# Optimization experiments

Measured on AMD Instinct MI355X. Metric: run time of the kernel, lower is better.

Reference implementation:

```python
import jax, jax.numpy as jnp
import numpy as np

D_MODEL = 1024
N_HEADS = 16
D_K = D_MODEL // N_HEADS
LOCAL_WINDOW = 128
GLOBAL_TOKENS = 16


def sparse_mask(seq_len):
    i = jnp.arange(seq_len)[:, None]
    j = jnp.arange(seq_len)[None, :]
    local = jnp.abs(i - j) <= LOCAL_WINDOW
    glob = (i < GLOBAL_TOKENS) | (j < GLOBAL_TOKENS)
    causal = j <= i
    return ((local | glob) & causal)[None, None]  # [1,1,S,S]


def setup_inputs() -> dict:
    key = jax.random.key(0)
    ks = jax.random.split(key, 11)
    B, S = 2, 2048
    std = 1.0 / np.sqrt(D_MODEL)
    inp = {
        'query': jax.random.normal(ks[0], (B, S, D_MODEL), jnp.float32),
        'key': jax.random.normal(ks[1], (B, S, D_MODEL), jnp.float32),
        'value': jax.random.normal(ks[2], (B, S, D_MODEL), jnp.float32),
        'w_q': jax.random.normal(ks[3], (D_MODEL, D_MODEL), jnp.float32) * std,
        'b_q': jnp.zeros((D_MODEL,), jnp.float32),
        'w_k': jax.random.normal(ks[4], (D_MODEL, D_MODEL), jnp.float32) * std,
        'b_k': jnp.zeros((D_MODEL,), jnp.float32),
        'w_v': jax.random.normal(ks[5], (D_MODEL, D_MODEL), jnp.float32) * std,
        'b_v': jnp.zeros((D_MODEL,), jnp.float32),
        'w_o': jax.random.normal(ks[6], (D_MODEL, D_MODEL), jnp.float32) * std,
        'b_o': jnp.zeros((D_MODEL,), jnp.float32),
    }
    return inp


def reference(query, key, value, w_q, b_q, w_k, b_k, w_v, b_v, w_o, b_o):
    B, S, _ = query.shape
    # project and split heads -> [B,H,S,d_k]
    def proj(x, w, b):
        y = x @ w.T + b
        return y.reshape(B, S, N_HEADS, D_K).transpose(0, 2, 1, 3)
    q = proj(query, w_q, b_q)
    k = proj(key, w_k, b_k)
    v = proj(value, w_v, b_v)
    scores = jnp.einsum('bhqd,bhkd->bhqk', q, k) / np.sqrt(D_K).astype(np.float32)
    mask = sparse_mask(S)
    scores = jnp.where(mask, scores, -jnp.inf)
    attn = jax.nn.softmax(scores, axis=-1)
    out = jnp.einsum('bhqk,bhkd->bhqd', attn, v)
    out = out.transpose(0, 2, 1, 3).reshape(B, S, D_MODEL)
    return out @ w_o.T + b_o
```

## Files before the change

kernel.cpp:

```cpp
#include <hip/hip_runtime.h>

typedef unsigned short u16;
typedef u16 u16x8 __attribute__((ext_vector_type(8)));
typedef __bf16 bf16x8 __attribute__((ext_vector_type(8)));
typedef float f32x4 __attribute__((ext_vector_type(4)));

#define MFMA16 __builtin_amdgcn_mfma_f32_16x16x32_bf16

__device__ __forceinline__ u16 f2bf(float f) {
  unsigned u = __builtin_bit_cast(unsigned, f);
  u += 0x7FFFu + ((u >> 16) & 1u);
  return (u16)(u >> 16);
}

__device__ __forceinline__ int swz(int row, int bcol) {
  return row * 128 + (bcol ^ ((row & 7) << 4));
}

__device__ __forceinline__ void gl16(const u16* g, u16* l) {
  __builtin_amdgcn_global_load_lds(
      (const __attribute__((address_space(1))) unsigned int*)g,
      (__attribute__((address_space(3))) unsigned int*)l, 16, 0, 0);
}

__device__ __forceinline__ void BARR() {
  asm volatile("" ::: "memory");
  __builtin_amdgcn_s_barrier();
  asm volatile("" ::: "memory");
}
#define VMCNT(n) asm volatile("s_waitcnt vmcnt(" #n ")" ::: "memory")
#define LGKM0 asm volatile("s_waitcnt lgkmcnt(0)" ::: "memory")

__global__ __launch_bounds__(256)
void cast_all(const float* __restrict__ q, const float* __restrict__ k,
              const float* __restrict__ v, const float* __restrict__ wq,
              const float* __restrict__ wk, const float* __restrict__ wv,
              const float* __restrict__ wo, u16* __restrict__ ws) {
  const long i = ((long)blockIdx.x * 256 + threadIdx.x) * 8;
  const float* s;
  u16* d;
  if (i < 12582912) {
    const int seg = (int)(i >> 22);
    const float* xs = (seg == 0) ? q : (seg == 1) ? k : v;
    s = xs + (i & 4194303);
    d = ws + 4194304 + i;
  } else {
    const long j = i - 12582912;
    const int seg = (int)(j >> 20);
    const float* wsrc = (seg == 0) ? wq : (seg == 1) ? wk : (seg == 2) ? wv : wo;
    s = wsrc + (j & 1048575);
    d = ws + j;
  }
  float4 v0 = *(const float4*)s;
  float4 v1 = *(const float4*)(s + 4);
  u16x8 p = {f2bf(v0.x), f2bf(v0.y), f2bf(v0.z), f2bf(v0.w),
             f2bf(v1.x), f2bf(v1.y), f2bf(v1.z), f2bf(v1.w)};
  *(u16x8*)d = p;
}

#define OSTGA(tt, c, j)                                                     \
  gl16(Ain + (m0 + (c)*64 + (w << 4) + (j)*8 + (lane >> 3)) * 1024 +        \
           (tt)*64 + (((lane & 7) ^ (lane >> 3)) << 3),                     \
       (u16*)(sb + (((tt)&1) << 15) + (c)*8192 + (w << 11) + ((j) << 10)))
#define OSTGB(tt, c, j)                                                     \
  gl16(W + (n0 + (c)*64 + (w << 4) + (j)*8 + (lane >> 3)) * 1024 +          \
           (tt)*64 + (((lane & 7) ^ (lane >> 3)) << 3),                     \
       (u16*)(sb + (((tt)&1) << 15) + 16384 + (c)*8192 + (w << 11) +        \
              ((j) << 10)))
#define OLDA()                                                              \
  _Pragma("unroll") for (int m = 0; m < 4; ++m) {                           \
    char* p = sb + bo + rowAb + m * 16 * 128;                               \
    af[0][m] = __builtin_bit_cast(bf16x8, *(const u16x8*)(p + colr0));      \
    af[1][m] = __builtin_bit_cast(bf16x8, *(const u16x8*)(p + colr1));      \
  }
#define OLDB(n)                                                             \
  {                                                                         \
    char* p = sb + bo + rowBb + (n)*16 * 128;                               \
    bf[0][n] = __builtin_bit_cast(bf16x8, *(const u16x8*)(p + colr0));      \
    bf[1][n] = __builtin_bit_cast(bf16x8, *(const u16x8*)(p + colr1));      \
  }
#define OFMA(nh)                                                            \
  __builtin_amdgcn_s_setprio(1);                                            \
  _Pragma("unroll") for (int m = 0; m < 4; ++m)                             \
  _Pragma("unroll") for (int n = 0; n < 2; ++n) {                           \
    acc[m][(nh)*2 + n] =                                                    \
        MFMA16(af[0][m], bf[0][(nh)*2 + n], acc[m][(nh)*2 + n], 0, 0, 0);   \
    acc[m][(nh)*2 + n] =                                                    \
        MFMA16(af[1][m], bf[1][(nh)*2 + n], acc[m][(nh)*2 + n], 0, 0, 0);   \
  }                                                                         \
  __builtin_amdgcn_s_setprio(0);

__device__ __forceinline__ void core128(const u16* __restrict__ Ain,
                                        const u16* __restrict__ W, int m0,
                                        int n0, char* sb,
                                        f32x4 (&acc)[4][4]) {
  const int tid = threadIdx.x, lane = tid & 63, w = tid >> 6;
  const int wm = w >> 1, wn = w & 1;
  const int r = lane & 15, g = lane >> 4;
  bf16x8 af[2][4], bf[2][4];

  const int colr0 = (g * 16) ^ ((r & 7) << 4);
  const int colr1 = (64 + g * 16) ^ ((r & 7) << 4);
  const int rowAb = (wm * 64 + r) * 128;
  const int rowBb = 16384 + (wn * 64 + r) * 128;

#pragma unroll
  for (int c = 0; c < 2; ++c) { OSTGA(0, c, 0); OSTGA(0, c, 1); }
#pragma unroll
  for (int c = 0; c < 2; ++c) { OSTGB(0, c, 0); OSTGB(0, c, 1); }
#pragma unroll
  for (int c = 0; c < 2; ++c) { OSTGA(1, c, 0); OSTGA(1, c, 1); }
  VMCNT(4);
  __builtin_amdgcn_s_barrier();
  asm volatile("" ::: "memory");

  for (int t = 0; t < 16; ++t) {
    const int bo = (t & 1) << 15;
    if (t < 15) { OSTGB(t + 1, 0, 0); OSTGB(t + 1, 0, 1); OSTGB(t + 1, 1, 0); OSTGB(t + 1, 1, 1); }
    OLDA();
    OLDB(0); OLDB(1);
    OFMA(0);
    BARR();
    if (t < 14) { OSTGA(t + 2, 0, 0); OSTGA(t + 2, 0, 1); OSTGA(t + 2, 1, 0); OSTGA(t + 2, 1, 1); }
    OLDB(2); OLDB(3);
    OFMA(1);
    if (t < 14) { VMCNT(4); } else if (t == 14) { VMCNT(0); }
    BARR();
  }
}

__global__ __launch_bounds__(256)
void qkv_gemm128(const u16* __restrict__ ws_in, const float* __restrict__ c0,
                 const float* __restrict__ c1, const float* __restrict__ c2,
                 u16* __restrict__ o0, u16* __restrict__ o1,
                 u16* __restrict__ o2) {
  const int bid = blockIdx.x;
  const int s = (bid & 7) * 96 + (bid >> 3);
  const int z = s >> 8;
  const int rem = s & 255;
  const int m0 = (rem >> 3) << 7, n0 = (rem & 7) << 7;

  const u16* __restrict__ Ain = ws_in + 4194304 + z * 4194304;
  const u16* __restrict__ W = ws_in + z * 1048576;
  const float* Bi = (z == 0) ? c0 : (z == 1) ? c1 : c2;
  u16* O = (z == 0) ? o0 : (z == 1) ? o1 : o2;

  const int tid = threadIdx.x, lane = tid & 63, w = tid >> 6;
  const int wm = w >> 1, wn = w & 1;
  const int r = lane & 15, g = lane >> 4;

  __shared__ u16 SH[32768];
  f32x4 acc[4][4] = {};
  core128(Ain, W, m0, n0, (char*)SH, acc);

#pragma unroll
  for (int n = 0; n < 4; ++n) {
    const int gn = n0 + wn * 64 + n * 16 + r;
    const int hh = gn >> 6, d = gn & 63;
    const float bv = Bi[gn];
#pragma unroll
    for (int m = 0; m < 4; ++m) {
#pragma unroll
      for (int q = 0; q < 4; ++q) {
        int gm = m0 + wm * 64 + m * 16 + g * 4 + q;
        int bb = gm >> 11, sIdx = gm & 2047;
        O[((bb * 16 + hh) * 2048 + sIdx) * 64 + d] = f2bf(acc[m][n][q] + bv);
      }
    }
  }
}

__global__ __launch_bounds__(256)
void out_gemm_p(const u16* __restrict__ Ain2, const u16* __restrict__ W2,
                const float* __restrict__ Bi, float* __restrict__ C) {
  const int bid = blockIdx.x;
  const int s = (bid & 7) * 32 + (bid >> 3);
  const int m0 = (s >> 3) << 7, n0 = (s & 7) << 7;

  const int tid = threadIdx.x, lane = tid & 63, w = tid >> 6;
  const int wm = w >> 1, wn = w & 1;
  const int r = lane & 15, g = lane >> 4;

  __shared__ u16 SH[32768];
  f32x4 acc[4][4] = {};
  core128(Ain2, W2, m0, n0, (char*)SH, acc);

#pragma unroll
  for (int m = 0; m < 4; ++m) {
#pragma unroll
    for (int n = 0; n < 4; ++n) {
      int gn = n0 + wn * 64 + n * 16 + r;
      float bv = Bi[gn];
#pragma unroll
      for (int q = 0; q < 4; ++q) {
        int gm = m0 + wm * 64 + m * 16 + g * 4 + q;
        C[gm * 1024 + gn] = acc[m][n][q] + bv;
      }
    }
  }
}

__global__ __launch_bounds__(256)
void attn_kernel(const u16* __restrict__ Q, const u16* __restrict__ K,
                 const u16* __restrict__ V, u16* __restrict__ O) {
  const int qt = blockIdx.x, h = blockIdx.y, b = blockIdx.z;
  const int tid = threadIdx.x, lane = tid & 63, w = tid >> 6;
  const int r = lane & 15, g = lane >> 4;
  const int q0 = qt * 64;
  const int base = (b * 16 + h) * 131072;
  const u16* Qb = Q + base;

  __shared__ u16 Ks[2][4096];
  __shared__ u16 Vt[2][4096];
  __shared__ u16 Pl[4608];

  bf16x8 qf[2];
  {
    const u16* qp = Qb + (q0 + w * 16 + r) * 64 + g * 8;
    qf[0] = __builtin_bit_cast(bf16x8, *(const u16x8*)qp);
    qf[1] = __builtin_bit_cast(bf16x8, *(const u16x8*)(qp + 32));
  }

  f32x4 acc[4] = {};
  float m_run[4] = {-1e30f, -1e30f, -1e30f, -1e30f};
  float l_run[4] = {};

  const int nt = (qt <= 3) ? (qt + 1) : 4;
  const int srow = tid >> 3, sc = (tid & 7) * 8;
  const u16* Kg = K + base + srow * 64 + sc;
  const u16* Vg = V + base + srow * 64 + sc;

  u16x8 krA[2], vrA[2], krB[2], vrB[2];
  krA[0] = *(const u16x8*)(Kg);
  krA[1] = *(const u16x8*)(Kg + 2048);
  vrA[0] = *(const u16x8*)(Vg);
  vrA[1] = *(const u16x8*)(Vg + 2048);

#pragma unroll
  for (int tix = 0; tix < 4; ++tix) {
    if (tix < nt) {
      const int j0 = ((tix == 0) ? 0 : ((qt <= 3) ? tix : (qt - 3 + tix))) * 64;
      const int bo = (tix & 1) * 8192;
      if ((tix & 1) == 0) {
#pragma unroll
        for (int i = 0; i < 2; ++i) {
          int row = i * 32 + srow;
          *(u16x8*)((char*)Ks + bo + swz(row, sc * 2)) = krA[i];
#pragma unroll
          for (int qq = 0; qq < 8; ++qq) {
            int d = sc + qq;
            *(u16*)((char*)Vt + bo + d * 128 + ((2 * row) ^ ((d & 7) << 4))) =
                vrA[i][qq];
          }
        }
      } else {
#pragma unroll
        for (int i = 0; i < 2; ++i) {
          int row = i * 32 + srow;
          *(u16x8*)((char*)Ks + bo + swz(row, sc * 2)) = krB[i];
#pragma unroll
          for (int qq = 0; qq < 8; ++qq) {
            int d = sc + qq;
            *(u16*)((char*)Vt + bo + d * 128 + ((2 * row) ^ ((d & 7) << 4))) =
                vrB[i][qq];
          }
        }
      }
      if (tix + 1 < nt) {
        const int jn = (((qt <= 3) ? (tix + 1) : (qt - 2 + tix)) * 64) * 64;
        if ((tix & 1) == 0) {
          krB[0] = *(const u16x8*)(Kg + jn);
          krB[1] = *(const u16x8*)(Kg + jn + 2048);
          vrB[0] = *(const u16x8*)(Vg + jn);
          vrB[1] = *(const u16x8*)(Vg + jn + 2048);
        } else {
          krA[0] = *(const u16x8*)(Kg + jn);
          krA[1] = *(const u16x8*)(Kg + jn + 2048);
          vrA[0] = *(const u16x8*)(Vg + jn);
          vrA[1] = *(const u16x8*)(Vg + jn + 2048);
        }
      }
      LGKM0;
      BARR();

      f32x4 S[4] = {};
#pragma unroll
      for (int kk = 0; kk < 2; ++kk)
#pragma unroll
        for (int n = 0; n < 4; ++n) {
          bf16x8 kf = __builtin_bit_cast(
              bf16x8, *(const u16x8*)((char*)Ks + bo +
                                      swz(n * 16 + r, kk * 64 + g * 16)));
          S[n] = MFMA16(qf[kk], kf, S[n], 0, 0, 0);
        }

      float mloc[4] = {-1e30f, -1e30f, -1e30f, -1e30f};
#pragma unroll
      for (int n = 0; n < 4; ++n) {
        int j = j0 + n * 16 + r;
#pragma unroll
        for (int q = 0; q < 4; ++q) {
          int i = q0 + w * 16 + g * 4 + q;
          bool ok = (j <= i) && (((i - j) <= 128) || (j < 16));
          float s = ok ? S[n][q] * 0.125f : -1e30f;
          S[n][q] = s;
          mloc[q] = fmaxf(mloc[q], s);
        }
      }
#pragma unroll
      for (int q = 0; q < 4; ++q)
#pragma unroll
        for (int off = 1; off < 16; off <<= 1)
          mloc[q] = fmaxf(mloc[q], __shfl_xor(mloc[q], off));

      float alpha[4], rsum[4] = {};
#pragma unroll
      for (int q = 0; q < 4; ++q) {
        float mn = fmaxf(m_run[q], mloc[q]);
        alpha[q] = __expf(m_run[q] - mn);
        m_run[q] = mn;
      }
#pragma unroll
      for (int n = 0; n < 4; ++n)
#pragma unroll
        for (int q = 0; q < 4; ++q) {
          float p = __expf(S[n][q] - m_run[q]);
          S[n][q] = p;
          rsum[q] += p;
        }
#pragma unroll
      for (int q = 0; q < 4; ++q) {
#pragma unroll
        for (int off = 1; off < 16; off <<= 1)
          rsum[q] += __shfl_xor(rsum[q], off);
        l_run[q] = l_run[q] * alpha[q] + rsum[q];
      }
#pragma unroll
      for (int n = 0; n < 4; ++n) {
        acc[n][0] *= alpha[0];
        acc[n][1] *= alpha[1];
        acc[n][2] *= alpha[2];
        acc[n][3] *= alpha[3];
      }

#pragma unroll
      for (int n = 0; n < 4; ++n)
#pragma unroll
        for (int q = 0; q < 4; ++q)
          *((u16*)((char*)Pl + w * 2304 + (g * 4 + q) * 144) + (n * 16 + r)) =
              f2bf(S[n][q]);

#pragma unroll
      for (int kk = 0; kk < 2; ++kk) {
        bf16x8 pf = __builtin_bit_cast(
            bf16x8, *(const u16x8*)((char*)Pl + w * 2304 + r * 144 + kk * 64 +
                                    g * 16));
#pragma unroll
        for (int n = 0; n < 4; ++n) {
          bf16x8 vf = __builtin_bit_cast(
              bf16x8, *(const u16x8*)((char*)Vt + bo +
                                      swz(n * 16 + r, kk * 64 + g * 16)));
          acc[n] = MFMA16(pf, vf, acc[n], 0, 0, 0);
        }
      }
    }
  }

#pragma unroll
  for (int n = 0; n < 4; ++n)
#pragma unroll
    for (int q = 0; q < 4; ++q) {
      int s = q0 + w * 16 + g * 4 + q;
      int d = n * 16 + r;
      O[(b * 2048 + s) * 1024 + h * 64 + d] = f2bf(acc[n][q] / l_run[q]);
    }
}

extern "C" void kernel_launch(void* const* d_in, const int* in_sizes, int n_in,
                              void* d_out, int out_size, void* d_ws,
                              size_t ws_size, hipStream_t stream) {
  const float* b_q = (const float*)d_in[4];
  const float* b_k = (const float*)d_in[6];
  const float* b_v = (const float*)d_in[8];
  const float* b_o = (const float*)d_in[10];

  u16* ws = (u16*)d_ws;
  u16* Qw = ws + 16777216;
  u16* Kw = ws + 20971520;
  u16* Vw = ws + 25165824;
  u16* Aw = ws + 4194304;

  cast_all<<<dim3(8192), dim3(256), 0, stream>>>(
      (const float*)d_in[0], (const float*)d_in[1], (const float*)d_in[2],
      (const float*)d_in[3], (const float*)d_in[5], (const float*)d_in[7],
      (const float*)d_in[9], ws);
  qkv_gemm128<<<dim3(768), dim3(256), 0, stream>>>(ws, b_q, b_k, b_v, Qw, Kw,
                                                   Vw);
  attn_kernel<<<dim3(32, 16, 2), dim3(256), 0, stream>>>(Qw, Kw, Vw, Aw);
  out_gemm_p<<<dim3(256), dim3(256), 0, stream>>>(Aw, ws + 3145728, b_o,
                                                  (float*)d_out);
}
```

Baseline: 92.72 us.

## Replace QKV projection GEMM with 256x256-tile 8-wave phased pipeline kernel

The QKV projection GEMM moves from 128x128 tiles with 4 waves (768 blocks) to 256x256 tiles with 8 waves (192 blocks) and 128KB of LDS. Each K-step is split into four quarter phases, with fine-grained global-to-LDS prefetch, lgkmcnt/vmcnt waits, sched barriers and setprio around the MFMA bursts. The larger tiles cut global and LDS traffic per FLOP. The cost is fewer blocks than CUs (192 vs 256), which can leave CUs idle and adds barrier overhead.

```diff
diff --git a/kernel.cpp b/kernel.cpp
--- a/kernel.cpp
+++ b/kernel.cpp
@@ -30,6 +30,9 @@
 }
 #define VMCNT(n) asm volatile("s_waitcnt vmcnt(" #n ")" ::: "memory")
 #define LGKM0 asm volatile("s_waitcnt lgkmcnt(0)" ::: "memory")
+#define LGKMH asm volatile("s_waitcnt lgkmcnt(8)" ::: "memory")
+#define SCHED0 __builtin_amdgcn_sched_barrier(0)
+#define FENCE asm volatile("" ::: "memory")
 
 __global__ __launch_bounds__(256)
 void cast_all(const float* __restrict__ q, const float* __restrict__ k,
@@ -58,6 +61,159 @@
   *(u16x8*)d = p;
 }
 
+__global__ __launch_bounds__(512)
+void qkv8ph(const u16* __restrict__ ws_in, const float* __restrict__ c0,
+            const float* __restrict__ c1, const float* __restrict__ c2,
+            u16* __restrict__ o0, u16* __restrict__ o1,
+            u16* __restrict__ o2) {
+  const int bid = blockIdx.x;
+  const int s = (bid & 7) * 24 + (bid >> 3);
+  const int z = s >> 6;
+  const int rem = s & 63;
+  const int m0 = (rem >> 2) << 8;
+  const int n0 = (rem & 3) << 8;
+
+  const u16* __restrict__ A = ws_in + 4194304 + z * 4194304;
+  const u16* __restrict__ W = ws_in + z * 1048576;
+  const float* Bi = (z == 0) ? c0 : (z == 1) ? c1 : c2;
+  u16* O = (z == 0) ? o0 : (z == 1) ? o1 : o2;
+
+  const int tid = threadIdx.x, lane = tid & 63, w = tid >> 6;
+  const int wm = w >> 2, wn = w & 3;
+  const int r = lane & 15, g = lane >> 4;
+
+  __shared__ u16 SH[65536];
+  char* sb = (char*)SH;
+
+  f32x4 acc[8][4] = {};
+  bf16x8 af[2][4], bf[2][2];
+
+  const int q8 = (w << 3) + (lane >> 3);
+  const int ce = ((lane & 7) ^ (lane >> 3)) << 3;
+
+#define SA(tt, h)                                                           \
+  {                                                                         \
+    FENCE;                                                                  \
+    gl16(A + (m0 + (h)*64 + q8) * 1024 + (tt)*64 + ce,                      \
+         (u16*)(sb + (((tt)&1) << 15) + ((h) << 14) + (w << 10)));          \
+    gl16(A + (m0 + 128 + (h)*64 + q8) * 1024 + (tt)*64 + ce,                \
+         (u16*)(sb + (((tt)&1) << 15) + ((h) << 14) + 8192 + (w << 10)));   \
+    FENCE;                                                                  \
+  }
+#define SB(tt, h)                                                           \
+  {                                                                         \
+    FENCE;                                                                  \
+    gl16(W + (n0 + (((q8 >> 5)) << 6) + (h)*32 + (q8 & 31)) * 1024 +        \
+             (tt)*64 + ce,                                                  \
+         (u16*)(sb + 65536 + (((tt)&1) << 15) + ((h) << 14) + (w << 10)));  \
+    gl16(W + (n0 + ((2 + (q8 >> 5)) << 6) + (h)*32 + (q8 & 31)) * 1024 +    \
+             (tt)*64 + ce,                                                  \
+         (u16*)(sb + 65536 + (((tt)&1) << 15) + ((h) << 14) + 8192 +        \
+                (w << 10)));                                                \
+    FENCE;                                                                  \
+  }
+
+  const int colk0 = (g * 16) ^ ((r & 7) << 4);
+  const int colk1 = (64 + g * 16) ^ ((r & 7) << 4);
+  const int rowA = (wm * 64 + r) * 128;
+  const int rowB = (wn * 32 + r) * 128;
+
+#define LDSA(h)                                                             \
+  _Pragma("unroll") for (int fi = 0; fi < 4; ++fi) {                        \
+    char* p = sb + bo + ((h) << 14) + rowA + fi * 2048;                     \
+    af[0][fi] = __builtin_bit_cast(bf16x8, *(const u16x8*)(p + colk0));     \
+    af[1][fi] = __builtin_bit_cast(bf16x8, *(const u16x8*)(p + colk1));     \
+  }
+#define LDSB(h)                                                             \
+  _Pragma("unroll") for (int n2 = 0; n2 < 2; ++n2) {                        \
+    char* p = sb + 65536 + bo + ((h) << 14) + rowB + n2 * 2048;             \
+    bf[0][n2] = __builtin_bit_cast(bf16x8, *(const u16x8*)(p + colk0));     \
+    bf[1][n2] = __builtin_bit_cast(bf16x8, *(const u16x8*)(p + colk1));     \
+  }
+#define FMAQ(mh, nh)                                                        \
+  __builtin_amdgcn_s_setprio(1);                                            \
+  _Pragma("unroll") for (int fi = 0; fi < 4; ++fi)                          \
+  _Pragma("unroll") for (int n2 = 0; n2 < 2; ++n2) {                        \
+    acc[(mh)*4 + fi][(nh)*2 + n2] = MFMA16(                                 \
+        af[0][fi], bf[0][n2], acc[(mh)*4 + fi][(nh)*2 + n2], 0, 0, 0);      \
+    acc[(mh)*4 + fi][(nh)*2 + n2] = MFMA16(                                 \
+        af[1][fi], bf[1][n2], acc[(mh)*4 + fi][(nh)*2 + n2], 0, 0, 0);      \
+  }                                                                         \
+  __builtin_amdgcn_s_setprio(0);
+
+  SA(0, 0);
+  SB(0, 0);
+  SB(0, 1);
+  SA(0, 1);
+  SA(1, 0);
+  SB(1, 0);
+  VMCNT(4);
+  __builtin_amdgcn_s_barrier();
+  FENCE;
+
+#pragma unroll 1
+  for (int t = 0; t < 16; ++t) {
+    const int bo = (t & 1) << 15;
+    if (t < 15) SB(t + 1, 1);
+    LDSA(0);
+    LDSB(0);
+    LGKMH;
+    BARR();
+    LGKM0;
+    SCHED0;
+    FMAQ(0, 0);
+    if (t < 15) { VMCNT(6); } else { VMCNT(2); }
+    BARR();
+    if (t < 14) SA(t + 2, 0);
+    LDSB(1);
+    BARR();
+    LGKM0;
+    SCHED0;
+    FMAQ(0, 1);
+    if (t < 14) { VMCNT(6); } else if (t == 14) { VMCNT(4); } else { VMCNT(0); }
+    BARR();
+    if (t < 15) SA(t + 1, 1);
+    LDSA(1);
+    LDSB(0);
+    LGKMH;
+    BARR();
+    LGKM0;
+    SCHED0;
+    FMAQ(1, 0);
+    if (t < 15) { VMCNT(6); }
+    BARR();
+    if (t < 14) SB(t + 2, 0);
+    LDSB(1);
+    BARR();
+    LGKM0;
+    SCHED0;
+    FMAQ(1, 1);
+    if (t < 14) { VMCNT(6); } else if (t == 14) { VMCNT(4); }
+    BARR();
+  }
+
+#pragma unroll
+  for (int n = 0; n < 4; ++n) {
+    const int gn = n0 + wn * 64 + (n >> 1) * 32 + (n & 1) * 16 + r;
+    const int hh = gn >> 6, d = gn & 63;
+    const float bv = Bi[gn];
+#pragma unroll
+    for (int m = 0; m < 8; ++m) {
+#pragma unroll
+      for (int q = 0; q < 4; ++q) {
+        int gm = m0 + wm * 128 + (m >> 2) * 64 + (m & 3) * 16 + g * 4 + q;
+        int bb = gm >> 11, sIdx = gm & 2047;
+        O[((bb * 16 + hh) * 2048 + sIdx) * 64 + d] = f2bf(acc[m][n][q] + bv);
+      }
+    }
+  }
+#undef SA
+#undef SB
+#undef LDSA
+#undef LDSB
+#undef FMAQ
+}
+
 #define OSTGA(tt, c, j)                                                     \
   gl16(Ain + (m0 + (c)*64 + (w << 4) + (j)*8 + (lane >> 3)) * 1024 +        \
            (tt)*64 + (((lane & 7) ^ (lane >> 3)) << 3),                     \
@@ -130,47 +286,6 @@
 }
 
 __global__ __launch_bounds__(256)
-void qkv_gemm128(const u16* __restrict__ ws_in, const float* __restrict__ c0,
-                 const float* __restrict__ c1, const float* __restrict__ c2,
-                 u16* __restrict__ o0, u16* __restrict__ o1,
-                 u16* __restrict__ o2) {
-  const int bid = blockIdx.x;
-  const int s = (bid & 7) * 96 + (bid >> 3);
-  const int z = s >> 8;
-  const int rem = s & 255;
-  const int m0 = (rem >> 3) << 7, n0 = (rem & 7) << 7;
-
-  const u16* __restrict__ Ain = ws_in + 4194304 + z * 4194304;
-  const u16* __restrict__ W = ws_in + z * 1048576;
-  const float* Bi = (z == 0) ? c0 : (z == 1) ? c1 : c2;
-  u16* O = (z == 0) ? o0 : (z == 1) ? o1 : o2;
-
-  const int tid = threadIdx.x, lane = tid & 63, w = tid >> 6;
-  const int wm = w >> 1, wn = w & 1;
-  const int r = lane & 15, g = lane >> 4;
-
-  __shared__ u16 SH[32768];
-  f32x4 acc[4][4] = {};
-  core128(Ain, W, m0, n0, (char*)SH, acc);
-
-#pragma unroll
-  for (int n = 0; n < 4; ++n) {
-    const int gn = n0 + wn * 64 + n * 16 + r;
-    const int hh = gn >> 6, d = gn & 63;
-    const float bv = Bi[gn];
-#pragma unroll
-    for (int m = 0; m < 4; ++m) {
-#pragma unroll
-      for (int q = 0; q < 4; ++q) {
-        int gm = m0 + wm * 64 + m * 16 + g * 4 + q;
-        int bb = gm >> 11, sIdx = gm & 2047;
-        O[((bb * 16 + hh) * 2048 + sIdx) * 64 + d] = f2bf(acc[m][n][q] + bv);
-      }
-    }
-  }
-}
-
-__global__ __launch_bounds__(256)
 void out_gemm_p(const u16* __restrict__ Ain2, const u16* __restrict__ W2,
                 const float* __restrict__ Bi, float* __restrict__ C) {
   const int bid = blockIdx.x;
@@ -394,8 +509,7 @@
       (const float*)d_in[0], (const float*)d_in[1], (const float*)d_in[2],
       (const float*)d_in[3], (const float*)d_in[5], (const float*)d_in[7],
       (const float*)d_in[9], ws);
-  qkv_gemm128<<<dim3(768), dim3(256), 0, stream>>>(ws, b_q, b_k, b_v, Qw, Kw,
-                                                   Vw);
+  qkv8ph<<<dim3(192), dim3(512), 0, stream>>>(ws, b_q, b_k, b_v, Qw, Kw, Vw);
   attn_kernel<<<dim3(32, 16, 2), dim3(256), 0, stream>>>(Qw, Kw, Vw, Aw);
   out_gemm_p<<<dim3(256), dim3(256), 0, stream>>>(Aw, ws + 3145728, b_o,
                                                   (float*)d_out);
```

Result: slower. 99.36 us (+7.2%).

## Use 128x64 tiles with custom pipelined mainloop for output projection GEMM

Applied to the files above, without the earlier changes.

Replaces the shared 128x128-tile core for the output projection with a dedicated 128x64-tile kernel, launching 512 blocks instead of 256 to fill more compute units on the 4096x1024x1024 GEMM. The new mainloop double-buffers A and B tiles in LDS with staggered async global-to-LDS loads, interleaving B loads with MFMAs and issuing A two steps ahead, and raises wave priority around MFMA groups. It trades reuse per block (more redundant A loads) for higher occupancy and overlap.

```diff
diff --git a/kernel.cpp b/kernel.cpp
--- a/kernel.cpp
+++ b/kernel.cpp
@@ -170,26 +170,86 @@
   }
 }
 
+#define ZSTGA(tt, j)                                                        \
+  gl16(Ain + (m0 + (w << 5) + (j)*8 + (lane >> 3)) * 1024 + (tt)*64 +       \
+           (((lane & 7) ^ (lane >> 3)) << 3),                               \
+       (u16*)(sb + ((tt)&1) * 24576 + (w << 12) + ((j) << 10)))
+#define ZSTGB(tt, j)                                                        \
+  gl16(W + (n0 + (w << 4) + (j)*8 + (lane >> 3)) * 1024 + (tt)*64 +         \
+           (((lane & 7) ^ (lane >> 3)) << 3),                               \
+       (u16*)(sb + ((tt)&1) * 24576 + 16384 + (w << 11) + ((j) << 10)))
+#define ZLDA()                                                              \
+  _Pragma("unroll") for (int m = 0; m < 4; ++m) {                           \
+    char* p = sb + bo + rowAb + m * 2048;                                   \
+    af[0][m] = __builtin_bit_cast(bf16x8, *(const u16x8*)(p + colr0));      \
+    af[1][m] = __builtin_bit_cast(bf16x8, *(const u16x8*)(p + colr1));      \
+  }
+#define ZLDB(n)                                                             \
+  {                                                                         \
+    char* p = sb + bo + rowBb + (n)*2048;                                   \
+    bf[0][n] = __builtin_bit_cast(bf16x8, *(const u16x8*)(p + colr0));      \
+    bf[1][n] = __builtin_bit_cast(bf16x8, *(const u16x8*)(p + colr1));      \
+  }
+#define ZFMA(n)                                                             \
+  __builtin_amdgcn_s_setprio(1);                                            \
+  _Pragma("unroll") for (int m = 0; m < 4; ++m) {                           \
+    acc[m][n] = MFMA16(af[0][m], bf[0][n], acc[m][n], 0, 0, 0);             \
+    acc[m][n] = MFMA16(af[1][m], bf[1][n], acc[m][n], 0, 0, 0);             \
+  }                                                                         \
+  __builtin_amdgcn_s_setprio(0);
+
 __global__ __launch_bounds__(256)
-void out_gemm_p(const u16* __restrict__ Ain2, const u16* __restrict__ W2,
+void out_gemm64(const u16* __restrict__ Ain, const u16* __restrict__ W,
                 const float* __restrict__ Bi, float* __restrict__ C) {
   const int bid = blockIdx.x;
-  const int s = (bid & 7) * 32 + (bid >> 3);
-  const int m0 = (s >> 3) << 7, n0 = (s & 7) << 7;
+  const int s = (bid & 7) * 64 + (bid >> 3);
+  const int m0 = (s >> 4) << 7;
+  const int n0 = (s & 15) << 6;
 
   const int tid = threadIdx.x, lane = tid & 63, w = tid >> 6;
   const int wm = w >> 1, wn = w & 1;
   const int r = lane & 15, g = lane >> 4;
 
-  __shared__ u16 SH[32768];
-  f32x4 acc[4][4] = {};
-  core128(Ain2, W2, m0, n0, (char*)SH, acc);
+  __shared__ u16 SH[24576];
+  char* sb = (char*)SH;
+
+  f32x4 acc[4][2] = {};
+  bf16x8 af[2][4], bf[2][2];
+
+  const int colr0 = (g * 16) ^ ((r & 7) << 4);
+  const int colr1 = (64 + g * 16) ^ ((r & 7) << 4);
+  const int rowAb = (wm * 64 + r) * 128;
+  const int rowBb = 16384 + (wn * 32 + r) * 128;
+
+#pragma unroll
+  for (int j = 0; j < 4; ++j) ZSTGA(0, j);
+#pragma unroll
+  for (int j = 0; j < 2; ++j) ZSTGB(0, j);
+#pragma unroll
+  for (int j = 0; j < 4; ++j) ZSTGA(1, j);
+  VMCNT(4);
+  __builtin_amdgcn_s_barrier();
+  asm volatile("" ::: "memory");
+
+  for (int t = 0; t < 16; ++t) {
+    const int bo = (t & 1) * 24576;
+    if (t < 15) { ZSTGB(t + 1, 0); ZSTGB(t + 1, 1); }
+    ZLDA();
+    ZLDB(0);
+    ZFMA(0);
+    BARR();
+    if (t < 14) { ZSTGA(t + 2, 0); ZSTGA(t + 2, 1); ZSTGA(t + 2, 2); ZSTGA(t + 2, 3); }
+    ZLDB(1);
+    ZFMA(1);
+    if (t < 14) { VMCNT(4); } else if (t == 14) { VMCNT(0); }
+    BARR();
+  }
 
 #pragma unroll
   for (int m = 0; m < 4; ++m) {
 #pragma unroll
-    for (int n = 0; n < 4; ++n) {
-      int gn = n0 + wn * 64 + n * 16 + r;
+    for (int n = 0; n < 2; ++n) {
+      int gn = n0 + wn * 32 + n * 16 + r;
       float bv = Bi[gn];
 #pragma unroll
       for (int q = 0; q < 4; ++q) {
@@ -397,6 +457,6 @@
   qkv_gemm128<<<dim3(768), dim3(256), 0, stream>>>(ws, b_q, b_k, b_v, Qw, Kw,
                                                    Vw);
   attn_kernel<<<dim3(32, 16, 2), dim3(256), 0, stream>>>(Qw, Kw, Vw, Aw);
-  out_gemm_p<<<dim3(256), dim3(256), 0, stream>>>(Aw, ws + 3145728, b_o,
+  out_gemm64<<<dim3(512), dim3(256), 0, stream>>>(Aw, ws + 3145728, b_o,
                                                   (float*)d_out);
 }
```

Measured after the change: 89.83 us. 1.03x faster.
